# Optimization experiments

Measured on AMD Instinct MI355X. Metric: run time of the kernel, lower is better.

Reference implementation:

```python
import jax, jax.numpy as jnp
import numpy as np

B, N, K, D, G = 4, 2048, 32, 64, 32
RADIUS = 0.8


def _linear_params(key, fin, fout):
    kw, kb = jax.random.split(key)
    lim = 1.0 / np.sqrt(fin)
    W = jax.random.uniform(kw, (fin, fout), jnp.float32, -lim, lim)
    b = jax.random.uniform(kb, (fout,), jnp.float32, -lim, lim)
    return W, b


def setup_inputs() -> dict:
    key = jax.random.key(0)
    ks = jax.random.split(key, 6)
    x = jax.random.normal(ks[0], (B, N, D), jnp.float32)
    pos = jax.random.uniform(ks[1], (B, N, 3), jnp.float32)
    W_first, b_first = _linear_params(ks[2], 3 * D, G)          # layer_first
    W1, b1 = _linear_params(ks[3], D + 1 * G, G)                # layers[0]
    W2, b2 = _linear_params(ks[4], D + 2 * G, G)                # layers[1]
    W_last, b_last = _linear_params(ks[5], D + 3 * G, G)        # layer_last
    return {"x": x, "pos": pos, "W_first": W_first, "b_first": b_first,
            "W1": W1, "b1": b1, "W2": W2, "b2": b2,
            "W_last": W_last, "b_last": b_last}


def ball_query(pos, radius, k):
    # pos: (B, N, 3). CUDA ball_query semantics: for each query point take the
    # first k points (in index order) with squared distance < radius^2; pad
    # remaining slots with the first found index. Self is always within radius.
    sq = jnp.sum(pos * pos, axis=-1)                            # (B, N)
    d2 = sq[:, :, None] + sq[:, None, :] - 2.0 * jnp.einsum("bnc,bmc->bnm", pos, pos)
    within = d2 < radius * radius                               # (B, N, N)
    n = pos.shape[1]
    cand = jnp.where(within, jnp.arange(n, dtype=jnp.int32)[None, None, :], n)
    idx = jnp.sort(cand, axis=-1)[..., :k]                      # first k hits, padded with n
    first = idx[..., :1]
    return jnp.where(idx == n, first, idx)                      # (B, N, K) int32


def reference(x, pos, W_first, b_first, W1, b1, W2, b2, W_last, b_last):
    idx = ball_query(pos, RADIUS, K)                            # (B, N, K)
    knn_feat = jax.vmap(lambda xb, ib: xb[ib])(x, idx)          # (B, N, K, D)
    x_tiled = jnp.broadcast_to(x[:, :, None, :], knn_feat.shape)
    edge_feat = jnp.concatenate([x_tiled, knn_feat, knn_feat - x_tiled], axis=-1)  # (B,N,K,3D)
    y = jnp.concatenate([jax.nn.relu(edge_feat @ W_first + b_first), x_tiled], axis=-1)  # G+D
    y = jnp.concatenate([jax.nn.relu(y @ W1 + b1), y], axis=-1)                     # 2G+D
    y = jnp.concatenate([jax.nn.relu(y @ W2 + b2), y], axis=-1)                     # 3G+D
    y = jnp.concatenate([y @ W_last + b_last, y], axis=-1)                          # 4G+D
    return jnp.max(y, axis=-2)                                  # (B, N, D + 4G)
```

## Files before the change

### kernel.cpp

```cpp
#include <hip/hip_runtime.h>
#include <hip/hip_bf16.h>

#define NB 4
#define NN 2048
#define KK 32
#define DD 64
#define R2C 0.64f

typedef __attribute__((ext_vector_type(8)))  short short8;
typedef __attribute__((ext_vector_type(16))) float f32x16;

__device__ __forceinline__ unsigned short f2bf(float f) {
    __hip_bfloat16 h = __float2bfloat16(f);
    return reinterpret_cast<unsigned short&>(h);
}

#define HSTRIDE 40

__device__ __forceinline__ void post_layer(const f32x16& acc, float bs,
                                           unsigned short* hl, int col, int g,
                                           float& mx, short8& f0, short8& f1) {
    float v[16];
#pragma unroll
    for (int p = 0; p < 16; ++p) v[p] = fmaxf(acc[p] + bs, 0.0f);
    float m = v[0];
#pragma unroll
    for (int p = 1; p < 16; ++p) m = fmaxf(m, v[p]);
    mx = fmaxf(m, __shfl_xor(m, 32));
#pragma unroll
    for (int p = 0; p < 16; ++p) {
        int r = (p & 3) + 8 * (p >> 2) + 4 * g;
        hl[r * HSTRIDE + col] = f2bf(v[p]);
    }
    const unsigned short* row = hl + col * HSTRIDE;
    f0 = *(const short8*)(row + 8 * g);
    f1 = *(const short8*)(row + 16 + 8 * g);
}

__device__ __forceinline__ short8 cvt8(const float* __restrict__ p) {
    float4 a = ((const float4*)p)[0];
    float4 b = ((const float4*)p)[1];
    short8 r;
    r[0] = (short)f2bf(a.x); r[1] = (short)f2bf(a.y); r[2] = (short)f2bf(a.z); r[3] = (short)f2bf(a.w);
    r[4] = (short)f2bf(b.x); r[5] = (short)f2bf(b.y); r[6] = (short)f2bf(b.z); r[7] = (short)f2bf(b.w);
    return r;
}

__device__ __forceinline__ void l1_mfma(const short8* hf, int lane, const short8* wl, f32x16& acc) {
#pragma unroll
    for (int p = 0; p < 16; ++p) acc[p] = 0.0f;
    acc = __builtin_amdgcn_mfma_f32_32x32x16_bf16(hf[0], wl[4 * 64 + lane], acc, 0, 0, 0);
    acc = __builtin_amdgcn_mfma_f32_32x32x16_bf16(hf[1], wl[5 * 64 + lane], acc, 0, 0, 0);
}

__device__ __forceinline__ void l2_mfma(const short8* h1, const short8* h0,
                                        int lane, const short8* wl, f32x16& acc) {
#pragma unroll
    for (int p = 0; p < 16; ++p) acc[p] = 0.0f;
    acc = __builtin_amdgcn_mfma_f32_32x32x16_bf16(h1[0], wl[6 * 64 + lane], acc, 0, 0, 0);
    acc = __builtin_amdgcn_mfma_f32_32x32x16_bf16(h1[1], wl[7 * 64 + lane], acc, 0, 0, 0);
    acc = __builtin_amdgcn_mfma_f32_32x32x16_bf16(h0[0], wl[8 * 64 + lane], acc, 0, 0, 0);
    acc = __builtin_amdgcn_mfma_f32_32x32x16_bf16(h0[1], wl[9 * 64 + lane], acc, 0, 0, 0);
}

__device__ __forceinline__ void l3_mfma(const short8* h2, const short8* h1, const short8* h0,
                                        int lane, const short8* wl, f32x16& acc) {
#pragma unroll
    for (int p = 0; p < 16; ++p) acc[p] = 0.0f;
    acc = __builtin_amdgcn_mfma_f32_32x32x16_bf16(h2[0], wl[10 * 64 + lane], acc, 0, 0, 0);
    acc = __builtin_amdgcn_mfma_f32_32x32x16_bf16(h2[1], wl[11 * 64 + lane], acc, 0, 0, 0);
    acc = __builtin_amdgcn_mfma_f32_32x32x16_bf16(h1[0], wl[12 * 64 + lane], acc, 0, 0, 0);
    acc = __builtin_amdgcn_mfma_f32_32x32x16_bf16(h1[1], wl[13 * 64 + lane], acc, 0, 0, 0);
    acc = __builtin_amdgcn_mfma_f32_32x32x16_bf16(h0[0], wl[14 * 64 + lane], acc, 0, 0, 0);
    acc = __builtin_amdgcn_mfma_f32_32x32x16_bf16(h0[1], wl[15 * 64 + lane], acc, 0, 0, 0);
}

__global__ __launch_bounds__(256, 4) void fused_kernel(const float* __restrict__ x,
                                                       const float* __restrict__ pos,
                                                       const float* __restrict__ Wf,
                                                       const float* __restrict__ bfv,
                                                       const float* __restrict__ W1,
                                                       const float* __restrict__ b1,
                                                       const float* __restrict__ W2,
                                                       const float* __restrict__ b2,
                                                       const float* __restrict__ Wl,
                                                       const float* __restrict__ bl,
                                                       float* __restrict__ out) {
    __shared__ unsigned short hlds[4][32 * HSTRIDE];
    __shared__ int nbrs[4][2][KK];
    __shared__ unsigned short lwf[16 * 64 * 8];
    int wid = threadIdx.x >> 6, lane = threadIdx.x & 63;
    int qp = __builtin_amdgcn_readfirstlane(blockIdx.x * 4 + wid);
    int q0 = qp << 1;
    int col = lane & 31, g = lane >> 5;
    int b = q0 >> 11, n0 = q0 & (NN - 1);

    for (int e = threadIdx.x; e < 1024; e += 256) {
        int f = e >> 6, l = e & 63;
        int c = l & 31, g2 = l >> 5;
        unsigned short* dst = lwf + (size_t)(f * 64 + l) * 8;
#pragma unroll
        for (int j = 0; j < 8; ++j) {
            int kl = 8 * g2 + j;
            float v;
            if (f < 4)       { int rr = 16 * f + kl;             v = Wf[(64 + rr) * 32 + c] + Wf[(128 + rr) * 32 + c]; }
            else if (f < 6)  { int rr = 16 * (f - 4) + kl;       v = W1[rr * 32 + c]; }
            else if (f < 8)  { int rr = 16 * (f - 6) + kl;       v = W2[rr * 32 + c]; }
            else if (f < 10) { int rr = 32 + 16 * (f - 8) + kl;  v = W2[rr * 32 + c]; }
            else if (f < 12) { int rr = 16 * (f - 10) + kl;      v = Wl[rr * 32 + c]; }
            else if (f < 14) { int rr = 32 + 16 * (f - 12) + kl; v = Wl[rr * 32 + c]; }
            else             { int rr = 64 + 16 * (f - 14) + kl; v = Wl[rr * 32 + c]; }
            dst[j] = f2bf(v);
        }
    }

    const float* xq0 = x + (size_t)q0 * DD;
    bool lo = lane < 32;
    int c0 = lane & 31;
    const float* pA1 = lo ? (Wf + c0) : (W1 + 32 * 32 + c0);
    const float* pA2 = lo ? (Wf + 128 * 32 + c0) : (W1 + 32 * 32 + c0);
    float sA = lo ? -1.0f : 0.0f;
    const float* pB1 = lo ? (W2 + 64 * 32 + c0) : (Wl + 96 * 32 + c0);
    float balA = lo ? bfv[c0] : b1[c0];
    float balB = lo ? b2[c0] : bl[c0];
    float aA[2] = {balA, balA};
    float aB[2] = {balB, balB};
#pragma unroll
    for (int j0 = 0; j0 < 16; ++j0) {
        float wa[4], wb[4];
#pragma unroll
        for (int jj = 0; jj < 4; ++jj) {
            int j = 4 * j0 + jj;
            wa[jj] = fmaf(sA, pA2[j * 32], pA1[j * 32]);
            wb[jj] = pB1[j * 32];
        }
#pragma unroll
        for (int t = 0; t < 2; ++t) {
            const float* xr = xq0 + t * DD + 4 * j0;
            float x0 = xr[0], x1 = xr[1], x2 = xr[2], x3 = xr[3];
            aA[t] = fmaf(x0, wa[0], aA[t]); aA[t] = fmaf(x1, wa[1], aA[t]);
            aA[t] = fmaf(x2, wa[2], aA[t]); aA[t] = fmaf(x3, wa[3], aA[t]);
            aB[t] = fmaf(x0, wb[0], aB[t]); aB[t] = fmaf(x1, wb[1], aB[t]);
            aB[t] = fmaf(x2, wb[2], aB[t]); aB[t] = fmaf(x3, wb[3], aB[t]);
        }
    }
    float bs0[2], bs1[2], bs2[2], bs3[2];
#pragma unroll
    for (int t = 0; t < 2; ++t) {
        bs0[t] = __shfl(aA[t], col, 64); bs1[t] = __shfl(aA[t], 32 + col, 64);
        bs2[t] = __shfl(aB[t], col, 64); bs3[t] = __shfl(aB[t], 32 + col, 64);
    }

    const float* pb = pos + (size_t)b * NN * 3;
    float qxv[2], qyv[2], qzv[2], sq4[2];
#pragma unroll
    for (int t = 0; t < 2; ++t) {
        int n = n0 + t;
        qxv[t] = pb[3 * n]; qyv[t] = pb[3 * n + 1]; qzv[t] = pb[3 * n + 2];
        sq4[t] = __fadd_rn(__fadd_rn(__fmul_rn(qxv[t], qxv[t]), __fmul_rn(qyv[t], qyv[t])),
                           __fmul_rn(qzv[t], qzv[t]));
    }
    int cnt[2] = {0, 0};
    unsigned long long ltmask = (1ULL << lane) - 1ULL;
    for (int m0 = 0; m0 < NN; m0 += 64) {
        if (cnt[0] >= KK && cnt[1] >= KK) break;
        int m = m0 + lane;
        float mx3 = pb[3 * m], my3 = pb[3 * m + 1], mz3 = pb[3 * m + 2];
        float sqm = __fadd_rn(__fadd_rn(__fmul_rn(mx3, mx3), __fmul_rn(my3, my3)), __fmul_rn(mz3, mz3));
#pragma unroll
        for (int t = 0; t < 2; ++t) {
            if (cnt[t] < KK) {
                float dot = __fadd_rn(__fadd_rn(__fmul_rn(qxv[t], mx3), __fmul_rn(qyv[t], my3)),
                                      __fmul_rn(qzv[t], mz3));
                float d2 = __fsub_rn(__fadd_rn(sq4[t], sqm), __fmul_rn(2.0f, dot));
                bool hit = d2 < R2C;
                unsigned long long mask = __ballot(hit);
                if (hit) {
                    int p = cnt[t] + (int)__popcll(mask & ltmask);
                    if (p < KK) nbrs[wid][t][p] = m;
                }
                cnt[t] = __builtin_amdgcn_readfirstlane(cnt[t] + (int)__popcll(mask));
            }
        }
    }
    int nbn[2];
#pragma unroll
    for (int t = 0; t < 2; ++t) nbn[t] = nbrs[wid][t][col < cnt[t] ? col : 0];

    short8 xk[2][4];
#pragma unroll
    for (int t = 0; t < 2; ++t) {
        const float* xrow = x + (size_t)(b * NN + nbn[t]) * DD + g * 8;
#pragma unroll
        for (int kf = 0; kf < 4; ++kf) xk[t][kf] = cvt8(xrow + kf * 16);
    }

    __syncthreads();
    const short8* wl = (const short8*)lwf;
    unsigned short* hl = hlds[wid];

    f32x16 a0, a1;
    float mx0[2], mx1[2], mx2[2];
    short8 h0f[2][2], h1f[2][2], h2f[2][2];

#pragma unroll
    for (int p = 0; p < 16; ++p) { a0[p] = 0.0f; a1[p] = 0.0f; }
#pragma unroll
    for (int f = 0; f < 4; ++f) a0 = __builtin_amdgcn_mfma_f32_32x32x16_bf16(xk[0][f], wl[f * 64 + lane], a0, 0, 0, 0);
#pragma unroll
    for (int f = 0; f < 4; ++f) a1 = __builtin_amdgcn_mfma_f32_32x32x16_bf16(xk[1][f], wl[f * 64 + lane], a1, 0, 0, 0);
    post_layer(a0, bs0[0], hl, col, g, mx0[0], h0f[0][0], h0f[0][1]);
    post_layer(a1, bs0[1], hl, col, g, mx0[1], h0f[1][0], h0f[1][1]);

    l1_mfma(h0f[0], lane, wl, a0);
    l1_mfma(h0f[1], lane, wl, a1);
    post_layer(a0, bs1[0], hl, col, g, mx1[0], h1f[0][0], h1f[0][1]);
    post_layer(a1, bs1[1], hl, col, g, mx1[1], h1f[1][0], h1f[1][1]);

    l2_mfma(h1f[0], h0f[0], lane, wl, a0);
    l2_mfma(h1f[1], h0f[1], lane, wl, a1);
    post_layer(a0, bs2[0], hl, col, g, mx2[0], h2f[0][0], h2f[0][1]);
    post_layer(a1, bs2[1], hl, col, g, mx2[1], h2f[1][0], h2f[1][1]);

    float m3[2];
    l3_mfma(h2f[0], h1f[0], h0f[0], lane, wl, a0);
    l3_mfma(h2f[1], h1f[1], h0f[1], lane, wl, a1);
    {
        float m = a0[0] + bs3[0];
#pragma unroll
        for (int p = 1; p < 16; ++p) m = fmaxf(m, a0[p] + bs3[0]);
        m3[0] = fmaxf(m, __shfl_xor(m, 32));
    }
    {
        float m = a1[0] + bs3[1];
#pragma unroll
        for (int p = 1; p < 16; ++p) m = fmaxf(m, a1[p] + bs3[1]);
        m3[1] = fmaxf(m, __shfl_xor(m, 32));
    }

#pragma unroll
    for (int t = 0; t < 2; ++t) {
        float* o = out + (size_t)(q0 + t) * 192;
        if (g == 0) {
            o[col]      = m3[t];
            o[32 + col] = mx2[t];
            o[64 + col] = mx1[t];
            o[96 + col] = mx0[t];
        }
        o[128 + lane] = xq0[t * DD + lane];
    }
}

extern "C" void kernel_launch(void* const* d_in, const int* in_sizes, int n_in,
                              void* d_out, int out_size, void* d_ws, size_t ws_size,
                              hipStream_t stream) {
    const float* x   = (const float*)d_in[0];
    const float* pos = (const float*)d_in[1];
    const float* Wf  = (const float*)d_in[2];
    const float* bf  = (const float*)d_in[3];
    const float* W1  = (const float*)d_in[4];
    const float* b1  = (const float*)d_in[5];
    const float* W2  = (const float*)d_in[6];
    const float* b2  = (const float*)d_in[7];
    const float* Wl  = (const float*)d_in[8];
    const float* bl  = (const float*)d_in[9];
    float* out = (float*)d_out;

    hipLaunchKernelGGL(fused_kernel, dim3(1024), dim3(256), 0, stream,
                       x, pos, Wf, bf, W1, b1, W2, b2, Wl, bl, out);
}
```

Before: 27.18 us.

## Precompute bf16 weight fragments and transposed x-weights in a prep kernel

Adds a small prep kernel that converts weights once per call into bf16 MFMA fragments and a transposed fp32 x-projection weight matrix with packed biases, stored in workspace. The main kernel then copies the prepared fragments into LDS with vector loads instead of converting and gathering weights in each of 1024 blocks, and reads x-projection weights as contiguous float4. This removes redundant per-block weight conversion and strided global loads, at the cost of an extra kernel launch and a dependency between the two launches.

```diff
diff --git a/kernel.cpp b/kernel.cpp
--- a/kernel.cpp
+++ b/kernel.cpp
@@ -15,90 +15,34 @@
     return reinterpret_cast<unsigned short&>(h);
 }
 
-#define HSTRIDE 40
-
-__device__ __forceinline__ void post_layer(const f32x16& acc, float bs,
-                                           unsigned short* hl, int col, int g,
-                                           float& mx, short8& f0, short8& f1) {
-    float v[16];
-#pragma unroll
-    for (int p = 0; p < 16; ++p) v[p] = fmaxf(acc[p] + bs, 0.0f);
-    float m = v[0];
-#pragma unroll
-    for (int p = 1; p < 16; ++p) m = fmaxf(m, v[p]);
-    mx = fmaxf(m, __shfl_xor(m, 32));
-#pragma unroll
-    for (int p = 0; p < 16; ++p) {
-        int r = (p & 3) + 8 * (p >> 2) + 4 * g;
-        hl[r * HSTRIDE + col] = f2bf(v[p]);
-    }
-    const unsigned short* row = hl + col * HSTRIDE;
-    f0 = *(const short8*)(row + 8 * g);
-    f1 = *(const short8*)(row + 16 + 8 * g);
-}
-
-__device__ __forceinline__ short8 cvt8(const float* __restrict__ p) {
-    float4 a = ((const float4*)p)[0];
-    float4 b = ((const float4*)p)[1];
-    short8 r;
-    r[0] = (short)f2bf(a.x); r[1] = (short)f2bf(a.y); r[2] = (short)f2bf(a.z); r[3] = (short)f2bf(a.w);
-    r[4] = (short)f2bf(b.x); r[5] = (short)f2bf(b.y); r[6] = (short)f2bf(b.z); r[7] = (short)f2bf(b.w);
-    return r;
-}
-
-__device__ __forceinline__ void l1_mfma(const short8* hf, int lane, const short8* wl, f32x16& acc) {
-#pragma unroll
-    for (int p = 0; p < 16; ++p) acc[p] = 0.0f;
-    acc = __builtin_amdgcn_mfma_f32_32x32x16_bf16(hf[0], wl[4 * 64 + lane], acc, 0, 0, 0);
-    acc = __builtin_amdgcn_mfma_f32_32x32x16_bf16(hf[1], wl[5 * 64 + lane], acc, 0, 0, 0);
-}
-
-__device__ __forceinline__ void l2_mfma(const short8* h1, const short8* h0,
-                                        int lane, const short8* wl, f32x16& acc) {
-#pragma unroll
-    for (int p = 0; p < 16; ++p) acc[p] = 0.0f;
-    acc = __builtin_amdgcn_mfma_f32_32x32x16_bf16(h1[0], wl[6 * 64 + lane], acc, 0, 0, 0);
-    acc = __builtin_amdgcn_mfma_f32_32x32x16_bf16(h1[1], wl[7 * 64 + lane], acc, 0, 0, 0);
-    acc = __builtin_amdgcn_mfma_f32_32x32x16_bf16(h0[0], wl[8 * 64 + lane], acc, 0, 0, 0);
-    acc = __builtin_amdgcn_mfma_f32_32x32x16_bf16(h0[1], wl[9 * 64 + lane], acc, 0, 0, 0);
-}
-
-__device__ __forceinline__ void l3_mfma(const short8* h2, const short8* h1, const short8* h0,
-                                        int lane, const short8* wl, f32x16& acc) {
-#pragma unroll
-    for (int p = 0; p < 16; ++p) acc[p] = 0.0f;
-    acc = __builtin_amdgcn_mfma_f32_32x32x16_bf16(h2[0], wl[10 * 64 + lane], acc, 0, 0, 0);
-    acc = __builtin_amdgcn_mfma_f32_32x32x16_bf16(h2[1], wl[11 * 64 + lane], acc, 0, 0, 0);
-    acc = __builtin_amdgcn_mfma_f32_32x32x16_bf16(h1[0], wl[12 * 64 + lane], acc, 0, 0, 0);
-    acc = __builtin_amdgcn_mfma_f32_32x32x16_bf16(h1[1], wl[13 * 64 + lane], acc, 0, 0, 0);
-    acc = __builtin_amdgcn_mfma_f32_32x32x16_bf16(h0[0], wl[14 * 64 + lane], acc, 0, 0, 0);
-    acc = __builtin_amdgcn_mfma_f32_32x32x16_bf16(h0[1], wl[15 * 64 + lane], acc, 0, 0, 0);
-}
-
-__global__ __launch_bounds__(256, 4) void fused_kernel(const float* __restrict__ x,
-                                                       const float* __restrict__ pos,
-                                                       const float* __restrict__ Wf,
-                                                       const float* __restrict__ bfv,
-                                                       const float* __restrict__ W1,
-                                                       const float* __restrict__ b1,
-                                                       const float* __restrict__ W2,
-                                                       const float* __restrict__ b2,
-                                                       const float* __restrict__ Wl,
-                                                       const float* __restrict__ bl,
-                                                       float* __restrict__ out) {
-    __shared__ unsigned short hlds[4][32 * HSTRIDE];
-    __shared__ int nbrs[4][2][KK];
-    __shared__ unsigned short lwf[16 * 64 * 8];
-    int wid = threadIdx.x >> 6, lane = threadIdx.x & 63;
-    int qp = __builtin_amdgcn_readfirstlane(blockIdx.x * 4 + wid);
-    int q0 = qp << 1;
-    int col = lane & 31, g = lane >> 5;
-    int b = q0 >> 11, n0 = q0 & (NN - 1);
-
-    for (int e = threadIdx.x; e < 1024; e += 256) {
-        int f = e >> 6, l = e & 63;
+__global__ __launch_bounds__(256) void prep_kernel(const float* __restrict__ Wf,
+                                                   const float* __restrict__ W1,
+                                                   const float* __restrict__ W2,
+                                                   const float* __restrict__ Wl,
+                                                   const float* __restrict__ bf,
+                                                   const float* __restrict__ b1,
+                                                   const float* __restrict__ b2,
+                                                   const float* __restrict__ bl,
+                                                   float* __restrict__ wxt,
+                                                   float* __restrict__ ball,
+                                                   unsigned short* __restrict__ wfrag) {
+    int blk = blockIdx.x;
+    if (blk < 32) {
+        int t = blk * 256 + threadIdx.x;
+        int ch = t >> 6, j = t & 63;
+        int L = ch >> 5, c = ch & 31;
+        float v;
+        if (L == 0)      v = Wf[j * 32 + c] - Wf[(128 + j) * 32 + c];
+        else if (L == 1) v = W1[(32 + j) * 32 + c];
+        else if (L == 2) v = W2[(64 + j) * 32 + c];
+        else             v = Wl[(96 + j) * 32 + c];
+        wxt[ch * 64 + j] = v;
+        if (j == 0) ball[ch] = (L == 0 ? bf[c] : L == 1 ? b1[c] : L == 2 ? b2[c] : bl[c]);
+    } else {
+        int t = (blk - 32) * 256 + threadIdx.x;
+        int f = t >> 6, l = t & 63;
         int c = l & 31, g2 = l >> 5;
-        unsigned short* dst = lwf + (size_t)(f * 64 + l) * 8;
+        unsigned short* dst = wfrag + (size_t)(f * 64 + l) * 8;
 #pragma unroll
         for (int j = 0; j < 8; ++j) {
             int kl = 8 * g2 + j;
@@ -113,35 +57,107 @@
             dst[j] = f2bf(v);
         }
     }
+}
+
+#define HSTRIDE 40
+
+__device__ __forceinline__ void post_layer(const f32x16& acc, float bs,
+                                           unsigned short* hl, int col, int g,
+                                           float& mx, short8& f0, short8& f1) {
+    float v[16];
+#pragma unroll
+    for (int p = 0; p < 16; ++p) v[p] = fmaxf(acc[p] + bs, 0.0f);
+    float m = v[0];
+#pragma unroll
+    for (int p = 1; p < 16; ++p) m = fmaxf(m, v[p]);
+    mx = fmaxf(m, __shfl_xor(m, 32));
+#pragma unroll
+    for (int p = 0; p < 16; ++p) {
+        int r = (p & 3) + 8 * (p >> 2) + 4 * g;
+        hl[r * HSTRIDE + col] = f2bf(v[p]);
+    }
+    const unsigned short* row = hl + col * HSTRIDE;
+    f0 = *(const short8*)(row + 8 * g);
+    f1 = *(const short8*)(row + 16 + 8 * g);
+}
+
+__device__ __forceinline__ short8 cvt8(const float* __restrict__ p) {
+    float4 a = ((const float4*)p)[0];
+    float4 b = ((const float4*)p)[1];
+    short8 r;
+    r[0] = (short)f2bf(a.x); r[1] = (short)f2bf(a.y); r[2] = (short)f2bf(a.z); r[3] = (short)f2bf(a.w);
+    r[4] = (short)f2bf(b.x); r[5] = (short)f2bf(b.y); r[6] = (short)f2bf(b.z); r[7] = (short)f2bf(b.w);
+    return r;
+}
+
+__device__ __forceinline__ void l1_mfma(const short8* hf, int lane, const short8* wl, f32x16& acc) {
+#pragma unroll
+    for (int p = 0; p < 16; ++p) acc[p] = 0.0f;
+    acc = __builtin_amdgcn_mfma_f32_32x32x16_bf16(hf[0], wl[4 * 64 + lane], acc, 0, 0, 0);
+    acc = __builtin_amdgcn_mfma_f32_32x32x16_bf16(hf[1], wl[5 * 64 + lane], acc, 0, 0, 0);
+}
+
+__device__ __forceinline__ void l2_mfma(const short8* h1, const short8* h0,
+                                        int lane, const short8* wl, f32x16& acc) {
+#pragma unroll
+    for (int p = 0; p < 16; ++p) acc[p] = 0.0f;
+    acc = __builtin_amdgcn_mfma_f32_32x32x16_bf16(h1[0], wl[6 * 64 + lane], acc, 0, 0, 0);
+    acc = __builtin_amdgcn_mfma_f32_32x32x16_bf16(h1[1], wl[7 * 64 + lane], acc, 0, 0, 0);
+    acc = __builtin_amdgcn_mfma_f32_32x32x16_bf16(h0[0], wl[8 * 64 + lane], acc, 0, 0, 0);
+    acc = __builtin_amdgcn_mfma_f32_32x32x16_bf16(h0[1], wl[9 * 64 + lane], acc, 0, 0, 0);
+}
+
+__device__ __forceinline__ void l3_mfma(const short8* h2, const short8* h1, const short8* h0,
+                                        int lane, const short8* wl, f32x16& acc) {
+#pragma unroll
+    for (int p = 0; p < 16; ++p) acc[p] = 0.0f;
+    acc = __builtin_amdgcn_mfma_f32_32x32x16_bf16(h2[0], wl[10 * 64 + lane], acc, 0, 0, 0);
+    acc = __builtin_amdgcn_mfma_f32_32x32x16_bf16(h2[1], wl[11 * 64 + lane], acc, 0, 0, 0);
+    acc = __builtin_amdgcn_mfma_f32_32x32x16_bf16(h1[0], wl[12 * 64 + lane], acc, 0, 0, 0);
+    acc = __builtin_amdgcn_mfma_f32_32x32x16_bf16(h1[1], wl[13 * 64 + lane], acc, 0, 0, 0);
+    acc = __builtin_amdgcn_mfma_f32_32x32x16_bf16(h0[0], wl[14 * 64 + lane], acc, 0, 0, 0);
+    acc = __builtin_amdgcn_mfma_f32_32x32x16_bf16(h0[1], wl[15 * 64 + lane], acc, 0, 0, 0);
+}
+
+__global__ __launch_bounds__(256, 4) void fused_kernel(const float* __restrict__ x,
+                                                       const float* __restrict__ pos,
+                                                       const float* __restrict__ wxt,
+                                                       const float* __restrict__ ball,
+                                                       const unsigned short* __restrict__ wfrag,
+                                                       float* __restrict__ out) {
+    __shared__ unsigned short hlds[4][32 * HSTRIDE];
+    __shared__ int nbrs[4][2][KK];
+    __shared__ unsigned short lwf[16 * 64 * 8];
+    int wid = threadIdx.x >> 6, lane = threadIdx.x & 63;
+    int qp = __builtin_amdgcn_readfirstlane(blockIdx.x * 4 + wid);
+    int q0 = qp << 1;
+    int col = lane & 31, g = lane >> 5;
+    int b = q0 >> 11, n0 = q0 & (NN - 1);
+
+    {
+        const float4* src = (const float4*)wfrag;
+        float4* dst = (float4*)lwf;
+#pragma unroll
+        for (int i = 0; i < 4; ++i) dst[threadIdx.x + 256 * i] = src[threadIdx.x + 256 * i];
+    }
 
     const float* xq0 = x + (size_t)q0 * DD;
-    bool lo = lane < 32;
-    int c0 = lane & 31;
-    const float* pA1 = lo ? (Wf + c0) : (W1 + 32 * 32 + c0);
-    const float* pA2 = lo ? (Wf + 128 * 32 + c0) : (W1 + 32 * 32 + c0);
-    float sA = lo ? -1.0f : 0.0f;
-    const float* pB1 = lo ? (W2 + 64 * 32 + c0) : (Wl + 96 * 32 + c0);
-    float balA = lo ? bfv[c0] : b1[c0];
-    float balB = lo ? b2[c0] : bl[c0];
+    float balA = ball[lane], balB = ball[64 + lane];
     float aA[2] = {balA, balA};
     float aB[2] = {balB, balB};
+    const float4* wA = (const float4*)(wxt + (size_t)lane * DD);
+    const float4* wB = (const float4*)(wxt + (size_t)(64 + lane) * DD);
 #pragma unroll
     for (int j0 = 0; j0 < 16; ++j0) {
-        float wa[4], wb[4];
-#pragma unroll
-        for (int jj = 0; jj < 4; ++jj) {
-            int j = 4 * j0 + jj;
-            wa[jj] = fmaf(sA, pA2[j * 32], pA1[j * 32]);
-            wb[jj] = pB1[j * 32];
-        }
+        float4 a4 = wA[j0], b4 = wB[j0];
 #pragma unroll
         for (int t = 0; t < 2; ++t) {
             const float* xr = xq0 + t * DD + 4 * j0;
             float x0 = xr[0], x1 = xr[1], x2 = xr[2], x3 = xr[3];
-            aA[t] = fmaf(x0, wa[0], aA[t]); aA[t] = fmaf(x1, wa[1], aA[t]);
-            aA[t] = fmaf(x2, wa[2], aA[t]); aA[t] = fmaf(x3, wa[3], aA[t]);
-            aB[t] = fmaf(x0, wb[0], aB[t]); aB[t] = fmaf(x1, wb[1], aB[t]);
-            aB[t] = fmaf(x2, wb[2], aB[t]); aB[t] = fmaf(x3, wb[3], aB[t]);
+            aA[t] = fmaf(x0, a4.x, aA[t]); aA[t] = fmaf(x1, a4.y, aA[t]);
+            aA[t] = fmaf(x2, a4.z, aA[t]); aA[t] = fmaf(x3, a4.w, aA[t]);
+            aB[t] = fmaf(x0, b4.x, aB[t]); aB[t] = fmaf(x1, b4.y, aB[t]);
+            aB[t] = fmaf(x2, b4.z, aB[t]); aB[t] = fmaf(x3, b4.w, aB[t]);
         }
     }
     float bs0[2], bs1[2], bs2[2], bs3[2];
@@ -266,6 +282,13 @@
     const float* bl  = (const float*)d_in[9];
     float* out = (float*)d_out;
 
+    char* ws = (char*)d_ws;
+    float*          wxt   = (float*)ws;
+    float*          ballp = (float*)(ws + 32768);
+    unsigned short* wfrag = (unsigned short*)(ws + 40960);
+
+    hipLaunchKernelGGL(prep_kernel, dim3(36), dim3(256), 0, stream,
+                       Wf, W1, W2, Wl, bf, b1, b2, bl, wxt, ballp, wfrag);
     hipLaunchKernelGGL(fused_kernel, dim3(1024), dim3(256), 0, stream,
-                       x, pos, Wf, bf, W1, b1, W2, b2, Wl, bl, out);
-}
+                       x, pos, wxt, ballp, wfrag, out);
+}
```

After: 36.49 us. +34.3%, slower.
